# Kernel optimization log

Measured on AMD Instinct MI355X. Metric: run time of the kernel, lower is better.

## Reference

```python
import jax, jax.numpy as jnp
import numpy as np

DIM = 64
HEADS = 4
N_NODES = 50000
N_EDGES = 800000
NEG_SLOPE = 0.2


def setup_inputs() -> dict:
    key = jax.random.key(0)
    k1, k2, k3, k4, k5 = jax.random.split(key, 5)
    meta_x = jax.random.normal(k1, (N_NODES, DIM), dtype=jnp.float32)
    meta_edge_index = jax.random.randint(k2, (2, N_EDGES), 0, N_NODES, dtype=jnp.int64)
    # GATConv params: shared source/dest Linear (no bias), per-head attention vecs, output bias.
    glorot = float(np.sqrt(2.0 / (DIM + HEADS * DIM)))
    W = jax.random.normal(k3, (DIM, HEADS * DIM), dtype=jnp.float32) * glorot  # x @ W
    att_src = jax.random.normal(k4, (1, HEADS, DIM), dtype=jnp.float32) * glorot
    att_dst = jax.random.normal(k5, (1, HEADS, DIM), dtype=jnp.float32) * glorot
    bias = jnp.zeros((DIM,), dtype=jnp.float32)
    return {"meta_x": meta_x, "meta_edge_index": meta_edge_index,
            "W": W, "att_src": att_src, "att_dst": att_dst, "bias": bias}


def reference(meta_x, meta_edge_index, W, att_src, att_dst, bias):
    N = meta_x.shape[0]
    # PyG GATConv default: add self-loops
    loops = jnp.arange(N, dtype=meta_edge_index.dtype)
    edge = jnp.concatenate([meta_edge_index, jnp.stack([loops, loops])], axis=1)
    src, dst = edge[0], edge[1]

    x = (meta_x @ W).reshape(N, HEADS, DIM)            # [N, H, C]
    a_src = jnp.sum(x * att_src, axis=-1)              # [N, H]
    a_dst = jnp.sum(x * att_dst, axis=-1)              # [N, H]

    logits = a_src[src] + a_dst[dst]                   # [E, H]
    logits = jax.nn.leaky_relu(logits, NEG_SLOPE)

    # segment softmax over edges grouped by destination node
    seg_max = jax.ops.segment_max(logits, dst, num_segments=N)   # [N, H]
    ex = jnp.exp(logits - seg_max[dst])
    seg_sum = jax.ops.segment_sum(ex, dst, num_segments=N)
    alpha = ex / (seg_sum[dst] + 1e-16)                # [E, H]

    msg = x[src] * alpha[:, :, None]                   # [E, H, C]
    out = jax.ops.segment_sum(msg, dst, num_segments=N)  # [N, H, C]
    # concat=False -> mean over heads, then bias
    return out.mean(axis=1) + bias
```

## Files before the change

kernel.cpp:

```cpp
#include <hip/hip_runtime.h>
#include <hip/hip_bf16.h>
#include <math.h>

#define MAXDEG 64
#define MAXCHUNK 6400

__device__ __forceinline__ float lrelu(float v) { return v > 0.0f ? v : 0.2f * v; }

__global__ void prep_kernel(int4* __restrict__ cnt4, int n4, int N,
                            const float* __restrict__ W, const float* __restrict__ att_src,
                            const float* __restrict__ att_dst, float* __restrict__ wsrc,
                            float* __restrict__ wdst) {
  int idx = blockIdx.x * 256 + threadIdx.x;
  for (int i = idx; i < n4; i += gridDim.x * 256) {
    int base = i * 4;
    int4 v;
    v.x = (base < N) ? 1 : 0;
    v.y = (base + 1 < N) ? 1 : 0;
    v.z = (base + 2 < N) ? 1 : 0;
    v.w = (base + 3 < N) ? 1 : 0;
    cnt4[i] = v;
  }
  if (blockIdx.x == 0) {
    int t = threadIdx.x;
    int h = t >> 6, k = t & 63;
    const float* wrow = W + (size_t)k * 256 + h * 64;
    const float* as = att_src + h * 64;
    const float* ad = att_dst + h * 64;
    float ss = 0.f, sd = 0.f;
#pragma unroll
    for (int c = 0; c < 64; ++c) {
      float w = wrow[c];
      ss = fmaf(w, as[c], ss);
      sd = fmaf(w, ad[c], sd);
    }
    wsrc[k * 4 + h] = ss;
    wdst[k * 4 + h] = sd;
  }
}

__global__ __launch_bounds__(256) void histpart_kernel(
    const int* __restrict__ ei, int* __restrict__ cntpart, int E, int N, int chunkN) {
  __shared__ int h[MAXCHUNK];
  int s = blockIdx.x >> 5, p = blockIdx.x & 31;
  int lo = s * chunkN;
  int hi = lo + chunkN; if (hi > N) hi = N;
  for (int i = threadIdx.x; i < chunkN; i += 256) h[i] = 0;
  __syncthreads();
  int E4 = E >> 2;
  int c0 = (int)(((long long)p * E4) >> 5);
  int c1 = (int)(((long long)(p + 1) * E4) >> 5);
  const int4* d4p = (const int4*)(ei + E);
  for (int i = c0 + threadIdx.x; i < c1; i += 256) {
    int4 d = d4p[i];
    if (d.x >= lo && d.x < hi) atomicAdd(&h[d.x - lo], 1);
    if (d.y >= lo && d.y < hi) atomicAdd(&h[d.y - lo], 1);
    if (d.z >= lo && d.z < hi) atomicAdd(&h[d.z - lo], 1);
    if (d.w >= lo && d.w < hi) atomicAdd(&h[d.w - lo], 1);
  }
  __syncthreads();
  int* out = cntpart + (size_t)blockIdx.x * chunkN;
  for (int i = threadIdx.x; i < chunkN; i += 256) out[i] = h[i];
}

__global__ void merge_kernel(const int* __restrict__ cntpart, int* __restrict__ cnt,
                             int N, int chunkN, int nbins) {
  int bin = blockIdx.x * 256 + threadIdx.x;
  if (bin >= nbins) return;
  if (bin < N) {
    int s = bin / chunkN;
    int i = bin - s * chunkN;
    const int* base = cntpart + (size_t)(s * 32) * chunkN + i;
    int sum = 1;
#pragma unroll
    for (int p = 0; p < 32; ++p) sum += base[(size_t)p * chunkN];
    cnt[bin] = sum;
  } else {
    cnt[bin] = 0;
  }
}

__global__ void nattn_kernel(const float* __restrict__ x, const float4* __restrict__ wsrc4,
                             const float4* __restrict__ wdst4, float4* __restrict__ asrc4,
                             float4* __restrict__ adst4, __hip_bfloat16* __restrict__ xh,
                             int N) {
  int lane = threadIdx.x & 63;
  int n = blockIdx.x * 4 + (threadIdx.x >> 6);
  if (n >= N) return;
  float xv = x[(size_t)n * 64 + lane];
  xh[(size_t)n * 64 + lane] = __float2bfloat16(xv);
  float4 ws = wsrc4[lane], wd = wdst4[lane];
  float s0 = xv * ws.x, s1 = xv * ws.y, s2 = xv * ws.z, s3 = xv * ws.w;
  float d0 = xv * wd.x, d1 = xv * wd.y, d2 = xv * wd.z, d3 = xv * wd.w;
#pragma unroll
  for (int m = 1; m < 64; m <<= 1) {
    s0 += __shfl_xor(s0, m, 64); s1 += __shfl_xor(s1, m, 64);
    s2 += __shfl_xor(s2, m, 64); s3 += __shfl_xor(s3, m, 64);
    d0 += __shfl_xor(d0, m, 64); d1 += __shfl_xor(d1, m, 64);
    d2 += __shfl_xor(d2, m, 64); d3 += __shfl_xor(d3, m, 64);
  }
  if (lane == 0) {
    asrc4[n] = make_float4(s0, s1, s2, s3);
    adst4[n] = make_float4(d0, d1, d2, d3);
  }
}

__global__ void hist_kernel(const int* __restrict__ ei, int* __restrict__ counts, int E) {
  int e = blockIdx.x * 256 + threadIdx.x;
  if (e >= E) return;
  atomicAdd(&counts[ei[(size_t)E + e]], 1);
}

__global__ void scatter_kernel(const int* __restrict__ ei, int* __restrict__ cursor,
                               int* __restrict__ src_sorted, int E, int N) {
  int e = blockIdx.x * 256 + threadIdx.x;
  int ET = E + N;
  if (e >= ET) return;
  int src, dst;
  if (e < E) {
    src = ei[e];
    dst = ei[(size_t)E + e];
  } else {
    src = dst = e - E;
  }
  int pos = atomicAdd(&cursor[dst], 1);
  src_sorted[pos] = src;
}

__global__ void scatter8_kernel(const int* __restrict__ ei, int* __restrict__ cursor,
                                int* __restrict__ srt, int E, int N) {
  int slice = blockIdx.x & 7;
  int bid = blockIdx.x >> 3;
  int nb = gridDim.x >> 3;
  int chunk = (N + 7) >> 3;
  int lo = slice * chunk;
  int hi = lo + chunk; if (hi > N) hi = N;
  int E4 = E >> 2;
  const int4* s4p = (const int4*)ei;
  const int4* d4p = (const int4*)(ei + E);
  int stride = nb * 256;
  for (int i = bid * 256 + threadIdx.x; i < E4; i += stride) {
    int4 d4 = d4p[i];
    bool bx = (d4.x >= lo && d4.x < hi), by = (d4.y >= lo && d4.y < hi);
    bool bz = (d4.z >= lo && d4.z < hi), bw = (d4.w >= lo && d4.w < hi);
    if (!(bx || by || bz || bw)) continue;
    int4 s4 = s4p[i];
    if (bx) { int p = atomicAdd(&cursor[d4.x], 1); srt[p] = s4.x; }
    if (by) { int p = atomicAdd(&cursor[d4.y], 1); srt[p] = s4.y; }
    if (bz) { int p = atomicAdd(&cursor[d4.z], 1); srt[p] = s4.z; }
    if (bw) { int p = atomicAdd(&cursor[d4.w], 1); srt[p] = s4.w; }
  }
  for (int n = lo + bid * 256 + threadIdx.x; n < hi; n += stride) {
    int p = atomicAdd(&cursor[n], 1);
    srt[p] = n;
  }
}

__global__ void scanABC_kernel(const int* __restrict__ cnt, int* __restrict__ row,
                               int* __restrict__ cur, int N, int ntiles) {
  __shared__ int tl[256];
  __shared__ int part[256];
  int b = blockIdx.x, t = threadIdx.x;
  int s = 0;
  if (t < ntiles) {
    const int4* c4 = (const int4*)cnt + t * 64;
    for (int i = 0; i < 64; ++i) {
      int4 v = c4[i];
      s += v.x + v.y + v.z + v.w;
    }
  }
  tl[t] = s;
  __syncthreads();
  for (int d = 1; d < 256; d <<= 1) {
    int u = (t >= d) ? tl[t - d] : 0;
    __syncthreads();
    tl[t] += u;
    __syncthreads();
  }
  int tileoff = (b == 0) ? 0 : tl[b - 1];
  int idx = b * 256 + t;
  int c = (idx < N) ? cnt[idx] : 0;
  part[t] = c;
  __syncthreads();
  for (int d = 1; d < 256; d <<= 1) {
    int u = (t >= d) ? part[t - d] : 0;
    __syncthreads();
    part[t] += u;
    __syncthreads();
  }
  int exc = part[t] - c + tileoff;
  if (idx < N) {
    row[idx] = exc;
    cur[idx] = exc;
    if (idx == N - 1) row[N] = exc + c;
  }
}

__global__ void scanA_kernel(const int* __restrict__ cnt, int* __restrict__ tsum, int N) {
  int b = blockIdx.x, t = threadIdx.x;
  int idx = b * 256 + t;
  int v = (idx < N) ? cnt[idx] : 0;
#pragma unroll
  for (int m = 1; m < 64; m <<= 1) v += __shfl_xor(v, m, 64);
  __shared__ int ws[4];
  if ((t & 63) == 0) ws[t >> 6] = v;
  __syncthreads();
  if (t == 0) tsum[b] = ws[0] + ws[1] + ws[2] + ws[3];
}

__global__ void scanB_kernel(int* __restrict__ tsum, int ntiles) {
  __shared__ int part[256];
  int t = threadIdx.x;
  int carry = 0;
  for (int b0 = 0; b0 < ntiles; b0 += 256) {
    int idx = b0 + t;
    int v = (idx < ntiles) ? tsum[idx] : 0;
    part[t] = v;
    __syncthreads();
    for (int d = 1; d < 256; d <<= 1) {
      int u = (t >= d) ? part[t - d] : 0;
      __syncthreads();
      part[t] += u;
      __syncthreads();
    }
    if (idx < ntiles) tsum[idx] = part[t] - v + carry;
    carry += part[255];
    __syncthreads();
  }
}

__global__ void scanC_kernel(const int* __restrict__ cnt, const int* __restrict__ tsum,
                             int* __restrict__ row, int* __restrict__ cur, int N) {
  __shared__ int part[256];
  int b = blockIdx.x, t = threadIdx.x;
  int idx = b * 256 + t;
  int c = (idx < N) ? cnt[idx] : 0;
  part[t] = c;
  __syncthreads();
  for (int d = 1; d < 256; d <<= 1) {
    int u = (t >= d) ? part[t - d] : 0;
    __syncthreads();
    part[t] += u;
    __syncthreads();
  }
  int exc = part[t] - c + tsum[b];
  if (idx < N) {
    row[idx] = exc;
    cur[idx] = exc;
    if (idx == N - 1) row[N] = exc + c;
  }
}

__global__ __launch_bounds__(256) void agg_kernel(
    const int* __restrict__ srt, const int* __restrict__ row,
    const float4* __restrict__ asrc4, const float4* __restrict__ adst4,
    const __hip_bfloat16* __restrict__ xh, __hip_bfloat16* __restrict__ agg, int N) {
  __shared__ float4 alL[4][MAXDEG];
  __shared__ int slL[4][MAXDEG];
  int t = threadIdx.x, w = t >> 6, lane = t & 63;
  int n = blockIdx.x * 4 + w;
  if (n >= N) return;
  int start = row[n], end = row[n + 1];
  int deg = end - start;
  float4 ad = adst4[n];
  float t0 = 0.f, t1 = 0.f, t2 = 0.f, t3 = 0.f;
  if (deg <= MAXDEG) {
    for (int b = 0; b < deg; b += 64) {
      if (b + lane < deg) {
        int sl = srt[start + b + lane];
        float4 as = asrc4[sl];
        float4 e;
        e.x = __expf(lrelu(as.x + ad.x));
        e.y = __expf(lrelu(as.y + ad.y));
        e.z = __expf(lrelu(as.z + ad.z));
        e.w = __expf(lrelu(as.w + ad.w));
        alL[w][b + lane] = e;
        slL[w][b + lane] = sl;
        t0 += e.x; t1 += e.y; t2 += e.z; t3 += e.w;
      }
    }
  } else {
    for (int b = start; b < end; b += 64) {
      int idx = b + lane;
      if (idx < end) {
        int sl = srt[idx];
        float4 as = asrc4[sl];
        t0 += __expf(lrelu(as.x + ad.x));
        t1 += __expf(lrelu(as.y + ad.y));
        t2 += __expf(lrelu(as.z + ad.z));
        t3 += __expf(lrelu(as.w + ad.w));
      }
    }
  }
#pragma unroll
  for (int m = 1; m < 64; m <<= 1) {
    t0 += __shfl_xor(t0, m, 64);
    t1 += __shfl_xor(t1, m, 64);
    t2 += __shfl_xor(t2, m, 64);
    t3 += __shfl_xor(t3, m, 64);
  }
  float r0 = 0.25f / (t0 + 1e-16f), r1 = 0.25f / (t1 + 1e-16f);
  float r2 = 0.25f / (t2 + 1e-16f), r3 = 0.25f / (t3 + 1e-16f);
  float a0 = 0.f, a1 = 0.f, a2 = 0.f, a3 = 0.f;
  if (deg <= MAXDEG) {
    int j = 0;
    for (; j + 4 <= deg; j += 4) {
      float4 e0 = alL[w][j], e1 = alL[w][j + 1], e2 = alL[w][j + 2], e3 = alL[w][j + 3];
      int q0 = slL[w][j], q1 = slL[w][j + 1], q2 = slL[w][j + 2], q3 = slL[w][j + 3];
      float v0 = __bfloat162float(xh[(size_t)q0 * 64 + lane]);
      float v1 = __bfloat162float(xh[(size_t)q1 * 64 + lane]);
      float v2 = __bfloat162float(xh[(size_t)q2 * 64 + lane]);
      float v3 = __bfloat162float(xh[(size_t)q3 * 64 + lane]);
      a0 = fmaf(e0.x, v0, a0); a1 = fmaf(e0.y, v0, a1);
      a2 = fmaf(e0.z, v0, a2); a3 = fmaf(e0.w, v0, a3);
      a0 = fmaf(e1.x, v1, a0); a1 = fmaf(e1.y, v1, a1);
      a2 = fmaf(e1.z, v1, a2); a3 = fmaf(e1.w, v1, a3);
      a0 = fmaf(e2.x, v2, a0); a1 = fmaf(e2.y, v2, a1);
      a2 = fmaf(e2.z, v2, a2); a3 = fmaf(e2.w, v2, a3);
      a0 = fmaf(e3.x, v3, a0); a1 = fmaf(e3.y, v3, a1);
      a2 = fmaf(e3.z, v3, a2); a3 = fmaf(e3.w, v3, a3);
    }
    for (; j < deg; ++j) {
      float4 e0 = alL[w][j];
      int q0 = slL[w][j];
      float v0 = __bfloat162float(xh[(size_t)q0 * 64 + lane]);
      a0 = fmaf(e0.x, v0, a0); a1 = fmaf(e0.y, v0, a1);
      a2 = fmaf(e0.z, v0, a2); a3 = fmaf(e0.w, v0, a3);
    }
  } else {
    for (int b = start; b < end; b += 64) {
      int cnt = end - b;
      if (cnt > 64) cnt = 64;
      int idx = b + lane;
      int sl = 0;
      float e0 = 0.f, e1 = 0.f, e2 = 0.f, e3 = 0.f;
      if (idx < end) {
        sl = srt[idx];
        float4 as = asrc4[sl];
        e0 = __expf(lrelu(as.x + ad.x));
        e1 = __expf(lrelu(as.y + ad.y));
        e2 = __expf(lrelu(as.z + ad.z));
        e3 = __expf(lrelu(as.w + ad.w));
      }
      for (int j = 0; j < cnt; ++j) {
        int sj = __shfl(sl, j, 64);
        float b0 = __shfl(e0, j, 64), b1 = __shfl(e1, j, 64);
        float b2 = __shfl(e2, j, 64), b3 = __shfl(e3, j, 64);
        float v = __bfloat162float(xh[(size_t)sj * 64 + lane]);
        a0 = fmaf(b0, v, a0); a1 = fmaf(b1, v, a1);
        a2 = fmaf(b2, v, a2); a3 = fmaf(b3, v, a3);
      }
    }
  }
  __hip_bfloat16* ao = agg + (size_t)n * 256;
  ao[lane] = __float2bfloat16(a0 * r0);
  ao[64 + lane] = __float2bfloat16(a1 * r1);
  ao[128 + lane] = __float2bfloat16(a2 * r2);
  ao[192 + lane] = __float2bfloat16(a3 * r3);
}

__global__ __launch_bounds__(256) void proj_kernel(
    const __hip_bfloat16* __restrict__ agg, const float* __restrict__ W,
    const float* __restrict__ bias, float* __restrict__ out, int N) {
  __shared__ float aggL[4][256];
  __shared__ float pL[4][4][64];
  int t = threadIdx.x, w = t >> 6, lane = t & 63;
  float Wreg[64];
#pragma unroll
  for (int k = 0; k < 64; ++k) Wreg[k] = W[(size_t)k * 256 + w * 64 + lane];
  float bv = bias[lane];
  int ngroups = (N + 3) >> 2;
  for (int g = blockIdx.x; g < ngroups; g += gridDim.x) {
    int n0 = g * 4;
    __syncthreads();
    {
      int nn = n0 + w;
      if (nn < N) {
        ushort4 u = ((const ushort4*)(agg + (size_t)nn * 256))[t & 63];
        float4 f;
        f.x = __bfloat162float(*(__hip_bfloat16*)&u.x);
        f.y = __bfloat162float(*(__hip_bfloat16*)&u.y);
        f.z = __bfloat162float(*(__hip_bfloat16*)&u.z);
        f.w = __bfloat162float(*(__hip_bfloat16*)&u.w);
        *(float4*)&aggL[w][(t & 63) * 4] = f;
      } else {
        *(float4*)&aggL[w][(t & 63) * 4] = make_float4(0.f, 0.f, 0.f, 0.f);
      }
    }
    __syncthreads();
    float acc0 = 0.f, acc1 = 0.f, acc2 = 0.f, acc3 = 0.f;
#pragma unroll
    for (int k4 = 0; k4 < 16; ++k4) {
      float4 av0 = *(const float4*)&aggL[0][w * 64 + k4 * 4];
      float4 av1 = *(const float4*)&aggL[1][w * 64 + k4 * 4];
      float4 av2 = *(const float4*)&aggL[2][w * 64 + k4 * 4];
      float4 av3 = *(const float4*)&aggL[3][w * 64 + k4 * 4];
      float w0 = Wreg[k4 * 4 + 0], w1 = Wreg[k4 * 4 + 1];
      float w2 = Wreg[k4 * 4 + 2], w3 = Wreg[k4 * 4 + 3];
      acc0 = fmaf(av0.x, w0, acc0); acc0 = fmaf(av0.y, w1, acc0);
      acc0 = fmaf(av0.z, w2, acc0); acc0 = fmaf(av0.w, w3, acc0);
      acc1 = fmaf(av1.x, w0, acc1); acc1 = fmaf(av1.y, w1, acc1);
      acc1 = fmaf(av1.z, w2, acc1); acc1 = fmaf(av1.w, w3, acc1);
      acc2 = fmaf(av2.x, w0, acc2); acc2 = fmaf(av2.y, w1, acc2);
      acc2 = fmaf(av2.z, w2, acc2); acc2 = fmaf(av2.w, w3, acc2);
      acc3 = fmaf(av3.x, w0, acc3); acc3 = fmaf(av3.y, w1, acc3);
      acc3 = fmaf(av3.z, w2, acc3); acc3 = fmaf(av3.w, w3, acc3);
    }
    pL[w][0][lane] = acc0;
    pL[w][1][lane] = acc1;
    pL[w][2][lane] = acc2;
    pL[w][3][lane] = acc3;
    __syncthreads();
    int nn = n0 + w;
    if (nn < N) {
      out[(size_t)nn * 64 + lane] = pL[0][w][lane] + pL[1][w][lane] +
                                    pL[2][w][lane] + pL[3][w][lane] + bv;
    }
  }
}

extern "C" void kernel_launch(void* const* d_in, const int* in_sizes, int n_in,
                              void* d_out, int out_size, void* d_ws, size_t ws_size,
                              hipStream_t stream) {
  const float* meta_x = (const float*)d_in[0];
  const int* ei = (const int*)d_in[1];
  const float* W = (const float*)d_in[2];
  const float* att_src = (const float*)d_in[3];
  const float* att_dst = (const float*)d_in[4];
  const float* bias = (const float*)d_in[5];
  float* out = (float*)d_out;

  int N = in_sizes[0] / 64;
  int E = in_sizes[1] / 2;
  int ET = E + N;
  int ntiles = (N + 255) / 256;
  int chunkN = (N + 7) / 8;

  char* ws = (char*)d_ws;
  size_t off = 0;
  auto alloc = [&](size_t bytes) {
    size_t o = off;
    off += (bytes + 255) & ~(size_t)255;
    return o;
  };
  size_t o_wsrc = alloc(64 * 4 * sizeof(float));
  size_t o_wdst = alloc(64 * 4 * sizeof(float));
  size_t o_asrc = alloc((size_t)N * 4 * sizeof(float));
  size_t o_adst = alloc((size_t)N * 4 * sizeof(float));
  size_t o_cnt = alloc((size_t)ntiles * 256 * sizeof(int));
  size_t o_row = alloc(((size_t)N + 1) * sizeof(int));
  size_t o_cur = alloc((size_t)N * sizeof(int));
  size_t o_srt = alloc((size_t)ET * sizeof(int));
  size_t o_ts = alloc((size_t)ntiles * sizeof(int));
  size_t o_cp = alloc((size_t)256 * chunkN * sizeof(int));
  size_t o_xh = alloc((size_t)N * 64 * sizeof(__hip_bfloat16));
  size_t o_agg = alloc((size_t)N * 256 * sizeof(__hip_bfloat16));
  (void)ws_size;

  float* wsrc = (float*)(ws + o_wsrc);
  float* wdst = (float*)(ws + o_wdst);
  float4* asrc4 = (float4*)(ws + o_asrc);
  float4* adst4 = (float4*)(ws + o_adst);
  int* cnt = (int*)(ws + o_cnt);
  int* row = (int*)(ws + o_row);
  int* cur = (int*)(ws + o_cur);
  int* srt = (int*)(ws + o_srt);
  int* tsum = (int*)(ws + o_ts);
  int* cntpart = (int*)(ws + o_cp);
  __hip_bfloat16* xh = (__hip_bfloat16*)(ws + o_xh);
  __hip_bfloat16* aggp = (__hip_bfloat16*)(ws + o_agg);

  int n4 = ntiles * 64;
  prep_kernel<<<64, 256, 0, stream>>>((int4*)cnt, n4, N, W, att_src, att_dst, wsrc, wdst);

  bool ldsHist = ((E & 3) == 0) && (chunkN <= MAXCHUNK);
  if (ldsHist) {
    histpart_kernel<<<256, 256, 0, stream>>>(ei, cntpart, E, N, chunkN);
    nattn_kernel<<<(N + 3) / 4, 256, 0, stream>>>(meta_x, (const float4*)wsrc,
                                                  (const float4*)wdst, asrc4, adst4, xh, N);
    merge_kernel<<<ntiles, 256, 0, stream>>>(cntpart, cnt, N, chunkN, ntiles * 256);
  } else {
    nattn_kernel<<<(N + 3) / 4, 256, 0, stream>>>(meta_x, (const float4*)wsrc,
                                                  (const float4*)wdst, asrc4, adst4, xh, N);
    hist_kernel<<<(E + 255) / 256, 256, 0, stream>>>(ei, cnt, E);
  }

  if (ntiles <= 256) {
    scanABC_kernel<<<ntiles, 256, 0, stream>>>(cnt, row, cur, N, ntiles);
  } else {
    scanA_kernel<<<ntiles, 256, 0, stream>>>(cnt, tsum, N);
    scanB_kernel<<<1, 256, 0, stream>>>(tsum, ntiles);
    scanC_kernel<<<ntiles, 256, 0, stream>>>(cnt, tsum, row, cur, N);
  }

  if ((E & 3) == 0) {
    scatter8_kernel<<<2048, 256, 0, stream>>>(ei, cur, srt, E, N);
  } else {
    scatter_kernel<<<(ET + 255) / 256, 256, 0, stream>>>(ei, cur, srt, E, N);
  }

  agg_kernel<<<(N + 3) / 4, 256, 0, stream>>>(srt, row, asrc4, adst4, xh, aggp, N);
  int ngroups = (N + 3) / 4;
  int pgrid = ngroups < 1024 ? ngroups : 1024;
  proj_kernel<<<pgrid, 256, 0, stream>>>(aggp, W, bias, out, N);
}
```

Measured before the change: 168.4 us.

## Scatter edges with LDS cursors seeded from per-partition histogram prefixes

The merge kernel now turns the per-partition histogram counts into exclusive prefixes in place. The new scatter kernel seeds a shared-memory cursor array from row offsets plus those prefixes, so each block places its edges with LDS atomics instead of global atomics on a shared cursor array. Each block also reads only its 1/32 slice of the edge list rather than striding over all edges. Self-loop entries are written directly by the scan kernel at each row start. The change targets global-atomic contention and redundant edge reads, at the cost of extra cntpart traffic and extra work inside the scan.

```diff
diff --git a/kernel.cpp b/kernel.cpp
--- a/kernel.cpp
+++ b/kernel.cpp
@@ -63,18 +63,22 @@
   for (int i = threadIdx.x; i < chunkN; i += 256) out[i] = h[i];
 }
 
-__global__ void merge_kernel(const int* __restrict__ cntpart, int* __restrict__ cnt,
-                             int N, int chunkN, int nbins) {
+__global__ void mergepfx_kernel(int* __restrict__ cntpart, int* __restrict__ cnt,
+                                int N, int chunkN, int nbins) {
   int bin = blockIdx.x * 256 + threadIdx.x;
   if (bin >= nbins) return;
   if (bin < N) {
     int s = bin / chunkN;
     int i = bin - s * chunkN;
-    const int* base = cntpart + (size_t)(s * 32) * chunkN + i;
-    int sum = 1;
-#pragma unroll
-    for (int p = 0; p < 32; ++p) sum += base[(size_t)p * chunkN];
-    cnt[bin] = sum;
+    int* base = cntpart + (size_t)(s * 32) * chunkN + i;
+    int run = 0;
+#pragma unroll
+    for (int p = 0; p < 32; ++p) {
+      int v = base[(size_t)p * chunkN];
+      base[(size_t)p * chunkN] = run;
+      run += v;
+    }
+    cnt[bin] = run + 1;
   } else {
     cnt[bin] = 0;
   }
@@ -127,37 +131,40 @@
   src_sorted[pos] = src;
 }
 
-__global__ void scatter8_kernel(const int* __restrict__ ei, int* __restrict__ cursor,
-                                int* __restrict__ srt, int E, int N) {
-  int slice = blockIdx.x & 7;
-  int bid = blockIdx.x >> 3;
-  int nb = gridDim.x >> 3;
-  int chunk = (N + 7) >> 3;
-  int lo = slice * chunk;
-  int hi = lo + chunk; if (hi > N) hi = N;
+__global__ __launch_bounds__(256) void scatterD_kernel(
+    const int* __restrict__ ei, const int* __restrict__ row,
+    const int* __restrict__ cntpart, int* __restrict__ srt, int E, int N, int chunkN) {
+  __shared__ int cur[MAXCHUNK];
+  int slice = blockIdx.x & 7, p = blockIdx.x >> 3;
+  int lo = slice * chunkN;
+  int hi = lo + chunkN; if (hi > N) hi = N;
+  const int* cp = cntpart + (size_t)(slice * 32 + p) * chunkN;
+  for (int i = threadIdx.x; i < chunkN; i += 256) {
+    int bin = lo + i;
+    cur[i] = (bin < N) ? row[bin] + 1 + cp[i] : 0;
+  }
+  __syncthreads();
   int E4 = E >> 2;
+  int c0 = (int)(((long long)p * E4) >> 5);
+  int c1 = (int)(((long long)(p + 1) * E4) >> 5);
   const int4* s4p = (const int4*)ei;
   const int4* d4p = (const int4*)(ei + E);
-  int stride = nb * 256;
-  for (int i = bid * 256 + threadIdx.x; i < E4; i += stride) {
-    int4 d4 = d4p[i];
-    bool bx = (d4.x >= lo && d4.x < hi), by = (d4.y >= lo && d4.y < hi);
-    bool bz = (d4.z >= lo && d4.z < hi), bw = (d4.w >= lo && d4.w < hi);
+  for (int i = c0 + threadIdx.x; i < c1; i += 256) {
+    int4 d = d4p[i];
+    bool bx = (d.x >= lo && d.x < hi), by = (d.y >= lo && d.y < hi);
+    bool bz = (d.z >= lo && d.z < hi), bw = (d.w >= lo && d.w < hi);
     if (!(bx || by || bz || bw)) continue;
-    int4 s4 = s4p[i];
-    if (bx) { int p = atomicAdd(&cursor[d4.x], 1); srt[p] = s4.x; }
-    if (by) { int p = atomicAdd(&cursor[d4.y], 1); srt[p] = s4.y; }
-    if (bz) { int p = atomicAdd(&cursor[d4.z], 1); srt[p] = s4.z; }
-    if (bw) { int p = atomicAdd(&cursor[d4.w], 1); srt[p] = s4.w; }
-  }
-  for (int n = lo + bid * 256 + threadIdx.x; n < hi; n += stride) {
-    int p = atomicAdd(&cursor[n], 1);
-    srt[p] = n;
+    int4 sv = s4p[i];
+    if (bx) { int q = atomicAdd(&cur[d.x - lo], 1); srt[q] = sv.x; }
+    if (by) { int q = atomicAdd(&cur[d.y - lo], 1); srt[q] = sv.y; }
+    if (bz) { int q = atomicAdd(&cur[d.z - lo], 1); srt[q] = sv.z; }
+    if (bw) { int q = atomicAdd(&cur[d.w - lo], 1); srt[q] = sv.w; }
   }
 }
 
 __global__ void scanABC_kernel(const int* __restrict__ cnt, int* __restrict__ row,
-                               int* __restrict__ cur, int N, int ntiles) {
+                               int* __restrict__ cur, int* __restrict__ srt,
+                               int N, int ntiles, int writeSelf) {
   __shared__ int tl[256];
   __shared__ int part[256];
   int b = blockIdx.x, t = threadIdx.x;
@@ -192,6 +199,7 @@
   if (idx < N) {
     row[idx] = exc;
     cur[idx] = exc;
+    if (writeSelf) srt[exc] = idx;
     if (idx == N - 1) row[N] = exc + c;
   }
 }
@@ -473,12 +481,12 @@
   int n4 = ntiles * 64;
   prep_kernel<<<64, 256, 0, stream>>>((int4*)cnt, n4, N, W, att_src, att_dst, wsrc, wdst);
 
-  bool ldsHist = ((E & 3) == 0) && (chunkN <= MAXCHUNK);
-  if (ldsHist) {
+  bool ldsPath = ((E & 3) == 0) && (chunkN <= MAXCHUNK);
+  if (ldsPath) {
     histpart_kernel<<<256, 256, 0, stream>>>(ei, cntpart, E, N, chunkN);
     nattn_kernel<<<(N + 3) / 4, 256, 0, stream>>>(meta_x, (const float4*)wsrc,
                                                   (const float4*)wdst, asrc4, adst4, xh, N);
-    merge_kernel<<<ntiles, 256, 0, stream>>>(cntpart, cnt, N, chunkN, ntiles * 256);
+    mergepfx_kernel<<<ntiles, 256, 0, stream>>>(cntpart, cnt, N, chunkN, ntiles * 256);
   } else {
     nattn_kernel<<<(N + 3) / 4, 256, 0, stream>>>(meta_x, (const float4*)wsrc,
                                                   (const float4*)wdst, asrc4, adst4, xh, N);
@@ -486,15 +494,16 @@
   }
 
   if (ntiles <= 256) {
-    scanABC_kernel<<<ntiles, 256, 0, stream>>>(cnt, row, cur, N, ntiles);
+    scanABC_kernel<<<ntiles, 256, 0, stream>>>(cnt, row, cur, srt, N, ntiles,
+                                               ldsPath ? 1 : 0);
   } else {
     scanA_kernel<<<ntiles, 256, 0, stream>>>(cnt, tsum, N);
     scanB_kernel<<<1, 256, 0, stream>>>(tsum, ntiles);
     scanC_kernel<<<ntiles, 256, 0, stream>>>(cnt, tsum, row, cur, N);
   }
 
-  if ((E & 3) == 0) {
-    scatter8_kernel<<<2048, 256, 0, stream>>>(ei, cur, srt, E, N);
+  if (ldsPath) {
+    scatterD_kernel<<<256, 256, 0, stream>>>(ei, row, cntpart, srt, E, N, chunkN);
   } else {
     scatter_kernel<<<(ET + 255) / 256, 256, 0, stream>>>(ei, cur, srt, E, N);
   }
```

Result: no change. 169.0 us (+0.3%).
